# Kernel tuning notes

Hardware: AMD Instinct MI355X
Metric: run time of the kernel (lower is better)

## Reference

```python
import jax, jax.numpy as jnp
import numpy as np

M, IN, OUT, R = 8192, 4096, 4096, 16  # tokens, in_features, out_features, lora rank


def setup_inputs() -> dict:
    key = jax.random.key(0)
    k = jax.random.split(key, 7)
    # symmetric int8 quantized activations and weights
    x = jax.random.randint(k[0], (M, IN), -127, 128, dtype=jnp.int8)
    weight = jax.random.randint(k[1], (OUT, IN), -127, 128, dtype=jnp.int8)
    # per-token activation scales and per-output-channel weight scales
    x_scales = jax.random.uniform(k[2], (M,), jnp.float32, 0.5, 1.5) / 127.0
    scales = jax.random.uniform(k[3], (OUT,), jnp.float32, 0.5, 1.5) / 127.0
    bias = jax.random.normal(k[4], (OUT,), jnp.float32)
    # module inits lora_a ~ N(0, 1/r); lora_b is zeros in the module but we use
    # small random values so the LoRA path is numerically exercised
    lora_a = jax.random.normal(k[5], (R, IN), jnp.float32) * (1.0 / R)
    lora_b = jax.random.normal(k[6], (OUT, R), jnp.float32) * 0.02
    return dict(x=x, weight=weight, bias=bias, x_scales=x_scales,
                scales=scales, lora_a=lora_a, lora_b=lora_b, fuse_gelu=1)


def reference(x, weight, bias, x_scales, scales, lora_a, lora_b, fuse_gelu):
    acc = jax.lax.dot_general(x, weight, (((1,), (1,)), ((), ())),
                              preferred_element_type=jnp.int32)
    # dequantize with outer product of per-token and per-channel scales
    main = acc.astype(jnp.float32) * x_scales[:, None] * scales[None, :]
    # LoRA correction on the dequantized activations: (x_deq @ A^T) @ B^T
    x_deq = x.astype(jnp.float32) * x_scales[:, None]          # [M, IN]
    lora = (x_deq @ lora_a.T) @ lora_b.T                        # [M, R] @ [R, OUT]
    out = main + lora + bias[None, :]
    if fuse_gelu:  # static Python flag
        out = jax.nn.gelu(out, approximate=True)  # tanh-approx GELU (CUDA fused path)
    return out
```

## Files before the change

### kernel.cpp

```cpp
#include <hip/hip_runtime.h>

#define M_DIM 8192
#define IN_DIM 4096
#define OUT_DIM 4096

typedef int   v4i  __attribute__((ext_vector_type(4)));
typedef int   v16i __attribute__((ext_vector_type(16)));
typedef short v8s  __attribute__((ext_vector_type(8)));
typedef float v4f  __attribute__((ext_vector_type(4)));
typedef float v16f __attribute__((ext_vector_type(16)));

static __device__ __forceinline__ int pack4(int a, int b, int c, int d) {
    return (a & 255) | ((b & 255) << 8) | ((c & 255) << 16) | ((d & 255) << 24);
}

static __device__ __forceinline__ short f2bf(float f) {
    unsigned u = __float_as_uint(f);
    u = (u + 0x7FFFu + ((u >> 16) & 1u)) >> 16;
    return (short)u;
}

static __device__ __forceinline__ short i2bf(int v) {
    float f = (float)v;
    return (short)(__float_as_uint(f) >> 16);
}

static __device__ __forceinline__ float gelu_tanh(float u) {
    float u2 = u * u;
    float p  = fmaf(u2, 0.0356774081f, 0.7978845608f);
    float v  = u * p;
    float e  = __builtin_amdgcn_exp2f(v * 2.8853900818f);
    return u - u * __builtin_amdgcn_rcpf(e + 1.0f);
}

static __device__ __forceinline__ void async_cp16(const signed char* g, signed char* l) {
    __builtin_amdgcn_global_load_lds((const __attribute__((address_space(1))) void*)g,
                                     (__attribute__((address_space(3))) void*)l, 16, 0, 0);
}


__global__ __launch_bounds__(256) void pack_a_kernel(const float* __restrict__ la,
                                                     short* __restrict__ a16,
                                                     float* __restrict__ T) {
    const int flat = blockIdx.x * 256 + threadIdx.x;
    size_t i = (size_t)flat * 8;
    const float4* p = (const float4*)(la + i);
    float4 a = p[0], b = p[1];
    v8s o;
    o[0] = f2bf(a.x); o[1] = f2bf(a.y); o[2] = f2bf(a.z); o[3] = f2bf(a.w);
    o[4] = f2bf(b.x); o[5] = f2bf(b.y); o[6] = f2bf(b.z); o[7] = f2bf(b.w);
    *(v8s*)(a16 + i) = o;
    float4 z = {0.f, 0.f, 0.f, 0.f};
    float4* tz = (float4*)(T + (size_t)flat * 16);
    tz[0] = z; tz[1] = z; tz[2] = z; tz[3] = z;
}

__global__ __launch_bounds__(256) void pack_w_kernel(const int* __restrict__ w,
                                                     signed char* __restrict__ w8t) {
    const int flat = blockIdx.x * 256 + threadIdx.x;
    const int l  = flat & 63;
    const int gp = (flat >> 6) & 15;
    const int kk = (flat >> 10) & 63;
    const int bn = flat >> 16;
    const int n = bn * 256 + ((gp >> 1) << 5) + (l & 31);
    const int k = kk * 64 + ((gp & 1) << 5) + ((l >> 5) << 4);
    const int4* p = (const int4*)(w + (size_t)n * IN_DIM + k);
    int4 a = p[0], b = p[1], c = p[2], d = p[3];
    int4 o;
    o.x = pack4(a.x, a.y, a.z, a.w);
    o.y = pack4(b.x, b.y, b.z, b.w);
    o.z = pack4(c.x, c.y, c.z, c.w);
    o.w = pack4(d.x, d.y, d.z, d.w);
    *(int4*)(w8t + (size_t)flat * 16) = o;
}

__global__ __launch_bounds__(256) void pack_x_lora_kernel(const int* __restrict__ x,
                                                          const short* __restrict__ a16,
                                                          signed char* __restrict__ x8t,
                                                          float* __restrict__ T) {
    __shared__ float red[4 * 256];
    const int tid = threadIdx.x;
    const int lane = tid & 63, wv = tid >> 6;
    const int fr = lane & 15, fq = lane >> 4;
    const int blk = blockIdx.x;
    const int m0 = (blk >> 2) * 16;
    const int ks = blk & 3;
    const int bm = m0 >> 8;
    const int g  = (m0 >> 5) & 7;
    const int l5 = (m0 & 16) + fr;
    const int row = m0 + fr;

    v4f acc = {0.f, 0.f, 0.f, 0.f};
#pragma unroll 4
    for (int kt = 0; kt < 8; ++kt) {
        const int k  = ks * 1024 + wv * 256 + kt * 32 + fq * 8;
        const int4* xp = (const int4*)(x + (size_t)row * IN_DIM + k);
        int4 a = xp[0], b = xp[1];
        const int kk = k >> 6, c = (k >> 4) & 3, j8 = (k >> 3) & 1;
        int2 pk = make_int2(pack4(a.x, a.y, a.z, a.w), pack4(b.x, b.y, b.z, b.w));
        *(int2*)(x8t + ((size_t)((bm * 64 + kk) * 16 + g * 2 + (c >> 1))) * 1024 +
                 ((c & 1) * 32 + l5) * 16 + j8 * 8) = pk;
        v8s xa;
        xa[0] = i2bf(a.x); xa[1] = i2bf(a.y); xa[2] = i2bf(a.z); xa[3] = i2bf(a.w);
        xa[4] = i2bf(b.x); xa[5] = i2bf(b.y); xa[6] = i2bf(b.z); xa[7] = i2bf(b.w);
        v8s aa = *(const v8s*)(a16 + (size_t)fr * IN_DIM + k);
        acc = __builtin_amdgcn_mfma_f32_16x16x32_bf16(xa, aa, acc, 0, 0, 0);
    }
    *(v4f*)&red[wv * 256 + lane * 4] = acc;
    __syncthreads();

    float s = red[tid] + red[256 + tid] + red[512 + tid] + red[768 + tid];
    const int sl = tid >> 2, j = tid & 3;
    const int r16 = ((sl >> 4) << 2) + j, col = sl & 15;
    atomicAdd(&T[(size_t)(m0 + r16) * 16 + col], s);
}

__global__ __launch_bounds__(256, 2) void q8_gemm_kernel(
    const signed char* __restrict__ x8t, const signed char* __restrict__ w8t,
    const float* __restrict__ Tp, const float* __restrict__ lbm,
    const float* __restrict__ bias, const float* __restrict__ xsc,
    const float* __restrict__ wsc, const int* __restrict__ gflag,
    float* __restrict__ out) {
    __shared__ __align__(16) signed char smem[73728];

    const int tid  = threadIdx.x;
    const int lane = tid & 63;
    const int wv   = tid >> 6;
    const int wm   = wv >> 1, wn = wv & 1;
    const int b   = blockIdx.x;
    const int xcd = b & 7, rr = b >> 3;
    const int bm  = xcd * 4 + (rr & 3);
    const int bn  = rr >> 2;

    const int lofs = lane * 16;
    const size_t toff = (size_t)tid * 16;
    const signed char* Asrc = x8t + (size_t)bm * (64 * 16 * 1024);
    const signed char* Bsrc = w8t + (size_t)(bn >> 1) * (64 * 16 * 1024) + (bn & 1) * 8192;

    v16i acc[4][2];
    {
        v16i z;
#pragma unroll
        for (int i = 0; i < 16; ++i) z[i] = 0;
#pragma unroll
        for (int mt = 0; mt < 4; ++mt)
#pragma unroll
            for (int nt = 0; nt < 2; ++nt) acc[mt][nt] = z;
    }

#pragma unroll
    for (int tt = 0; tt < 2; ++tt) {
        const signed char* gA = Asrc + (size_t)tt * 16384 + toff;
        const signed char* gB = Bsrc + (size_t)tt * 16384 + toff;
        signed char* sA = smem + tt * 24576 + (wv << 10);
        signed char* sB = sA + 16384;
        async_cp16(gA,         sA);
        async_cp16(gA + 4096,  sA + 4096);
        async_cp16(gA + 8192,  sA + 8192);
        async_cp16(gA + 12288, sA + 12288);
        async_cp16(gB,         sB);
        async_cp16(gB + 4096,  sB + 4096);
    }
    asm volatile("s_waitcnt vmcnt(6)" ::: "memory");
    __builtin_amdgcn_s_barrier();

    int cur = 0;
    for (int t = 0; t < 64; ++t) {
        const signed char* Ab = smem + cur * 24576;
        const signed char* Bb = Ab + 16384;
        const int sb = (cur == 0) ? 2 : cur - 1;
        signed char* sA = smem + sb * 24576 + (wv << 10);
        signed char* sB = sA + 16384;
        const signed char* gA = Asrc + (size_t)(t + 2) * 16384 + toff;
        const signed char* gB = Bsrc + (size_t)(t + 2) * 16384 + toff;
        const bool pf = (t < 62);

        v4i a0, a1, a2, a3, b0, b1;

        a0 = *(const v4i*)(Ab + ((wm * 4 + 0) * 2 + 0) * 1024 + lofs);
        a1 = *(const v4i*)(Ab + ((wm * 4 + 1) * 2 + 0) * 1024 + lofs);
        a2 = *(const v4i*)(Ab + ((wm * 4 + 2) * 2 + 0) * 1024 + lofs);
        a3 = *(const v4i*)(Ab + ((wm * 4 + 3) * 2 + 0) * 1024 + lofs);
        b0 = *(const v4i*)(Bb + ((wn * 2 + 0) * 2 + 0) * 1024 + lofs);
        b1 = *(const v4i*)(Bb + ((wn * 2 + 1) * 2 + 0) * 1024 + lofs);
        if (pf) {
            async_cp16(gA,        sA);
            async_cp16(gA + 4096, sA + 4096);
            async_cp16(gB,        sB);
        }
        __builtin_amdgcn_s_barrier();
        __builtin_amdgcn_s_setprio(1);
        acc[0][0] = __builtin_amdgcn_mfma_i32_32x32x32_i8(a0, b0, acc[0][0], 0, 0, 0);
        acc[0][1] = __builtin_amdgcn_mfma_i32_32x32x32_i8(a0, b1, acc[0][1], 0, 0, 0);
        acc[1][0] = __builtin_amdgcn_mfma_i32_32x32x32_i8(a1, b0, acc[1][0], 0, 0, 0);
        acc[1][1] = __builtin_amdgcn_mfma_i32_32x32x32_i8(a1, b1, acc[1][1], 0, 0, 0);
        acc[2][0] = __builtin_amdgcn_mfma_i32_32x32x32_i8(a2, b0, acc[2][0], 0, 0, 0);
        acc[2][1] = __builtin_amdgcn_mfma_i32_32x32x32_i8(a2, b1, acc[2][1], 0, 0, 0);
        acc[3][0] = __builtin_amdgcn_mfma_i32_32x32x32_i8(a3, b0, acc[3][0], 0, 0, 0);
        acc[3][1] = __builtin_amdgcn_mfma_i32_32x32x32_i8(a3, b1, acc[3][1], 0, 0, 0);
        __builtin_amdgcn_s_setprio(0);

        a0 = *(const v4i*)(Ab + ((wm * 4 + 0) * 2 + 1) * 1024 + lofs);
        a1 = *(const v4i*)(Ab + ((wm * 4 + 1) * 2 + 1) * 1024 + lofs);
        a2 = *(const v4i*)(Ab + ((wm * 4 + 2) * 2 + 1) * 1024 + lofs);
        a3 = *(const v4i*)(Ab + ((wm * 4 + 3) * 2 + 1) * 1024 + lofs);
        b0 = *(const v4i*)(Bb + ((wn * 2 + 0) * 2 + 1) * 1024 + lofs);
        b1 = *(const v4i*)(Bb + ((wn * 2 + 1) * 2 + 1) * 1024 + lofs);
        if (pf) {
            async_cp16(gA + 8192,  sA + 8192);
            async_cp16(gA + 12288, sA + 12288);
            async_cp16(gB + 4096,  sB + 4096);
        }
        __builtin_amdgcn_s_barrier();
        __builtin_amdgcn_s_setprio(1);
        acc[0][0] = __builtin_amdgcn_mfma_i32_32x32x32_i8(a0, b0, acc[0][0], 0, 0, 0);
        acc[0][1] = __builtin_amdgcn_mfma_i32_32x32x32_i8(a0, b1, acc[0][1], 0, 0, 0);
        acc[1][0] = __builtin_amdgcn_mfma_i32_32x32x32_i8(a1, b0, acc[1][0], 0, 0, 0);
        acc[1][1] = __builtin_amdgcn_mfma_i32_32x32x32_i8(a1, b1, acc[1][1], 0, 0, 0);
        acc[2][0] = __builtin_amdgcn_mfma_i32_32x32x32_i8(a2, b0, acc[2][0], 0, 0, 0);
        acc[2][1] = __builtin_amdgcn_mfma_i32_32x32x32_i8(a2, b1, acc[2][1], 0, 0, 0);
        acc[3][0] = __builtin_amdgcn_mfma_i32_32x32x32_i8(a3, b0, acc[3][0], 0, 0, 0);
        acc[3][1] = __builtin_amdgcn_mfma_i32_32x32x32_i8(a3, b1, acc[3][1], 0, 0, 0);
        __builtin_amdgcn_s_setprio(0);

        if (pf) {
            asm volatile("s_waitcnt vmcnt(6)" ::: "memory");
        } else if (t == 62) {
            asm volatile("s_waitcnt vmcnt(0)" ::: "memory");
        }
        if (t < 63) __builtin_amdgcn_s_barrier();
        cur = (cur == 2) ? 0 : cur + 1;
    }

    const int mbase = bm * 256 + wm * 128;
    const int nbase = bn * 128 + wn * 64;
    const int l31 = lane & 31, lh = lane >> 5;
    const bool dg = (*gflag) != 0;

    v8s tf[4], bf[2];
#pragma unroll
    for (int mt = 0; mt < 4; ++mt) {
        const float* t0 = Tp + (size_t)(mbase + mt * 32 + l31) * 16 + lh * 8;
        v8s v;
#pragma unroll
        for (int j = 0; j < 8; ++j) v[j] = f2bf(t0[j]);
        tf[mt] = v;
    }
#pragma unroll
    for (int nt = 0; nt < 2; ++nt) {
        const float* bp = lbm + (size_t)(nbase + nt * 32 + l31) * 16 + lh * 8;
        v8s v;
#pragma unroll
        for (int j = 0; j < 8; ++j) v[j] = f2bf(bp[j]);
        bf[nt] = v;
    }
    float wsa[2], bba[2];
#pragma unroll
    for (int nt = 0; nt < 2; ++nt) {
        const int col = nbase + nt * 32 + l31;
        wsa[nt] = wsc[col];
        bba[nt] = bias[col];
    }

#pragma unroll
    for (int mt = 0; mt < 4; ++mt) {
        const int rowb = mbase + mt * 32 + lh * 4;
        float4 xs0 = *(const float4*)(xsc + rowb);
        float4 xs1 = *(const float4*)(xsc + rowb + 8);
        float4 xs2 = *(const float4*)(xsc + rowb + 16);
        float4 xs3 = *(const float4*)(xsc + rowb + 24);
        float xsv[16] = {xs0.x, xs0.y, xs0.z, xs0.w, xs1.x, xs1.y, xs1.z, xs1.w,
                         xs2.x, xs2.y, xs2.z, xs2.w, xs3.x, xs3.y, xs3.z, xs3.w};
#pragma unroll
        for (int nt = 0; nt < 2; ++nt) {
            v16f fa;
#pragma unroll
            for (int i = 0; i < 16; ++i) fa[i] = (float)acc[mt][nt][i] * wsa[nt];
            fa = __builtin_amdgcn_mfma_f32_32x32x16_bf16(tf[mt], bf[nt], fa, 0, 0, 0);
            const int col = nbase + nt * 32 + l31;
#pragma unroll
            for (int r = 0; r < 16; ++r) {
                float u = fmaf(xsv[r], fa[r], bba[nt]);
                if (dg) u = gelu_tanh(u);
                out[(size_t)(rowb + (r & 3) + 8 * (r >> 2)) * OUT_DIM + col] = u;
            }
        }
    }
}

extern "C" void kernel_launch(void* const* d_in, const int* in_sizes, int n_in,
                              void* d_out, int out_size, void* d_ws, size_t ws_size,
                              hipStream_t stream) {
    const int*   x     = (const int*)d_in[0];
    const int*   wt    = (const int*)d_in[1];
    const float* bias  = (const float*)d_in[2];
    const float* xsc   = (const float*)d_in[3];
    const float* wsc   = (const float*)d_in[4];
    const float* la    = (const float*)d_in[5];
    const float* lb    = (const float*)d_in[6];
    const int*   gflag = (const int*)d_in[7];
    float* out = (float*)d_out;

    signed char* x8t = (signed char*)d_ws;
    signed char* w8t = x8t + (size_t)M_DIM * IN_DIM;
    float* T = (float*)(w8t + (size_t)OUT_DIM * IN_DIM);
    short* a16 = (short*)w8t;

    pack_a_kernel<<<16 * IN_DIM / (8 * 256), 256, 0, stream>>>(la, a16, T);
    pack_x_lora_kernel<<<(M_DIM / 16) * 4, 256, 0, stream>>>(x, a16, x8t, T);
    pack_w_kernel<<<(size_t)OUT_DIM * IN_DIM / (16 * 256), 256, 0, stream>>>(wt, w8t);
    q8_gemm_kernel<<<(M_DIM / 256) * (OUT_DIM / 128), 256, 0, stream>>>(
        x8t, w8t, T, lb, bias, xsc, wsc, gflag, out);
}
```

Baseline: 423.9 us.

## Merge x/LoRA and weight packing into one launch, convert lora_a inline

Replaces the separate lora_a packing kernel, x-pack/LoRA kernel and weight-pack kernel with a small zeroing kernel plus one combined kernel. Blocks below 2048 pack activations and compute the LoRA projection, and the remaining blocks pack weights. lora_a is now read as fp32 and converted to bf16 inside the LoRA loop instead of being pre-packed. The aim is to cut launch overhead and let the two packing jobs overlap, at the cost of redundant fp32 reads and conversions of lora_a in every block.

Measured after the change: 418.7 us. Within noise of the previous version (-1.2%).

```diff
diff --git a/kernel.cpp b/kernel.cpp
--- a/kernel.cpp
+++ b/kernel.cpp
@@ -39,80 +39,77 @@
 }
 
 
-__global__ __launch_bounds__(256) void pack_a_kernel(const float* __restrict__ la,
-                                                     short* __restrict__ a16,
-                                                     float* __restrict__ T) {
+__global__ __launch_bounds__(256) void zero_t_kernel(float* __restrict__ T) {
     const int flat = blockIdx.x * 256 + threadIdx.x;
-    size_t i = (size_t)flat * 8;
-    const float4* p = (const float4*)(la + i);
-    float4 a = p[0], b = p[1];
-    v8s o;
-    o[0] = f2bf(a.x); o[1] = f2bf(a.y); o[2] = f2bf(a.z); o[3] = f2bf(a.w);
-    o[4] = f2bf(b.x); o[5] = f2bf(b.y); o[6] = f2bf(b.z); o[7] = f2bf(b.w);
-    *(v8s*)(a16 + i) = o;
     float4 z = {0.f, 0.f, 0.f, 0.f};
-    float4* tz = (float4*)(T + (size_t)flat * 16);
-    tz[0] = z; tz[1] = z; tz[2] = z; tz[3] = z;
-}
-
-__global__ __launch_bounds__(256) void pack_w_kernel(const int* __restrict__ w,
-                                                     signed char* __restrict__ w8t) {
-    const int flat = blockIdx.x * 256 + threadIdx.x;
-    const int l  = flat & 63;
-    const int gp = (flat >> 6) & 15;
-    const int kk = (flat >> 10) & 63;
-    const int bn = flat >> 16;
-    const int n = bn * 256 + ((gp >> 1) << 5) + (l & 31);
-    const int k = kk * 64 + ((gp & 1) << 5) + ((l >> 5) << 4);
-    const int4* p = (const int4*)(w + (size_t)n * IN_DIM + k);
-    int4 a = p[0], b = p[1], c = p[2], d = p[3];
-    int4 o;
-    o.x = pack4(a.x, a.y, a.z, a.w);
-    o.y = pack4(b.x, b.y, b.z, b.w);
-    o.z = pack4(c.x, c.y, c.z, c.w);
-    o.w = pack4(d.x, d.y, d.z, d.w);
-    *(int4*)(w8t + (size_t)flat * 16) = o;
-}
-
-__global__ __launch_bounds__(256) void pack_x_lora_kernel(const int* __restrict__ x,
-                                                          const short* __restrict__ a16,
-                                                          signed char* __restrict__ x8t,
-                                                          float* __restrict__ T) {
+    float4* tz = (float4*)(T + (size_t)flat * 8);
+    tz[0] = z; tz[1] = z;
+}
+
+__global__ __launch_bounds__(256) void pack_all_kernel(const int* __restrict__ x,
+                                                       const float* __restrict__ la,
+                                                       signed char* __restrict__ x8t,
+                                                       float* __restrict__ T,
+                                                       const int* __restrict__ w,
+                                                       signed char* __restrict__ w8t) {
     __shared__ float red[4 * 256];
+    const int b = blockIdx.x;
     const int tid = threadIdx.x;
-    const int lane = tid & 63, wv = tid >> 6;
-    const int fr = lane & 15, fq = lane >> 4;
-    const int blk = blockIdx.x;
-    const int m0 = (blk >> 2) * 16;
-    const int ks = blk & 3;
-    const int bm = m0 >> 8;
-    const int g  = (m0 >> 5) & 7;
-    const int l5 = (m0 & 16) + fr;
-    const int row = m0 + fr;
-
-    v4f acc = {0.f, 0.f, 0.f, 0.f};
+    if (b < 2048) {
+        const int lane = tid & 63, wv = tid >> 6;
+        const int fr = lane & 15, fq = lane >> 4;
+        const int m0 = (b >> 2) * 16;
+        const int ks = b & 3;
+        const int bm = m0 >> 8;
+        const int g  = (m0 >> 5) & 7;
+        const int l5 = (m0 & 16) + fr;
+        const int row = m0 + fr;
+
+        v4f acc = {0.f, 0.f, 0.f, 0.f};
 #pragma unroll 4
-    for (int kt = 0; kt < 8; ++kt) {
-        const int k  = ks * 1024 + wv * 256 + kt * 32 + fq * 8;
-        const int4* xp = (const int4*)(x + (size_t)row * IN_DIM + k);
-        int4 a = xp[0], b = xp[1];
-        const int kk = k >> 6, c = (k >> 4) & 3, j8 = (k >> 3) & 1;
-        int2 pk = make_int2(pack4(a.x, a.y, a.z, a.w), pack4(b.x, b.y, b.z, b.w));
-        *(int2*)(x8t + ((size_t)((bm * 64 + kk) * 16 + g * 2 + (c >> 1))) * 1024 +
-                 ((c & 1) * 32 + l5) * 16 + j8 * 8) = pk;
-        v8s xa;
-        xa[0] = i2bf(a.x); xa[1] = i2bf(a.y); xa[2] = i2bf(a.z); xa[3] = i2bf(a.w);
-        xa[4] = i2bf(b.x); xa[5] = i2bf(b.y); xa[6] = i2bf(b.z); xa[7] = i2bf(b.w);
-        v8s aa = *(const v8s*)(a16 + (size_t)fr * IN_DIM + k);
-        acc = __builtin_amdgcn_mfma_f32_16x16x32_bf16(xa, aa, acc, 0, 0, 0);
-    }
-    *(v4f*)&red[wv * 256 + lane * 4] = acc;
-    __syncthreads();
-
-    float s = red[tid] + red[256 + tid] + red[512 + tid] + red[768 + tid];
-    const int sl = tid >> 2, j = tid & 3;
-    const int r16 = ((sl >> 4) << 2) + j, col = sl & 15;
-    atomicAdd(&T[(size_t)(m0 + r16) * 16 + col], s);
+        for (int kt = 0; kt < 8; ++kt) {
+            const int k  = ks * 1024 + wv * 256 + kt * 32 + fq * 8;
+            const int4* xp = (const int4*)(x + (size_t)row * IN_DIM + k);
+            int4 a = xp[0], bb = xp[1];
+            const int kk = k >> 6, c = (k >> 4) & 3, j8 = (k >> 3) & 1;
+            int2 pk = make_int2(pack4(a.x, a.y, a.z, a.w), pack4(bb.x, bb.y, bb.z, bb.w));
+            *(int2*)(x8t + ((size_t)((bm * 64 + kk) * 16 + g * 2 + (c >> 1))) * 1024 +
+                     ((c & 1) * 32 + l5) * 16 + j8 * 8) = pk;
+            v8s xa;
+            xa[0] = i2bf(a.x);  xa[1] = i2bf(a.y);  xa[2] = i2bf(a.z);  xa[3] = i2bf(a.w);
+            xa[4] = i2bf(bb.x); xa[5] = i2bf(bb.y); xa[6] = i2bf(bb.z); xa[7] = i2bf(bb.w);
+            const float* ap = la + (size_t)fr * IN_DIM + k;
+            float4 af0 = *(const float4*)(ap);
+            float4 af1 = *(const float4*)(ap + 4);
+            v8s aa;
+            aa[0] = f2bf(af0.x); aa[1] = f2bf(af0.y); aa[2] = f2bf(af0.z); aa[3] = f2bf(af0.w);
+            aa[4] = f2bf(af1.x); aa[5] = f2bf(af1.y); aa[6] = f2bf(af1.z); aa[7] = f2bf(af1.w);
+            acc = __builtin_amdgcn_mfma_f32_16x16x32_bf16(xa, aa, acc, 0, 0, 0);
+        }
+        *(v4f*)&red[wv * 256 + lane * 4] = acc;
+        __syncthreads();
+
+        float s = red[tid] + red[256 + tid] + red[512 + tid] + red[768 + tid];
+        const int sl = tid >> 2, j = tid & 3;
+        const int r16 = ((sl >> 4) << 2) + j, col = sl & 15;
+        atomicAdd(&T[(size_t)(m0 + r16) * 16 + col], s);
+    } else {
+        const int flat = (b - 2048) * 256 + tid;
+        const int l  = flat & 63;
+        const int gp = (flat >> 6) & 15;
+        const int kk = (flat >> 10) & 63;
+        const int bn = flat >> 16;
+        const int n = bn * 256 + ((gp >> 1) << 5) + (l & 31);
+        const int k = kk * 64 + ((gp & 1) << 5) + ((l >> 5) << 4);
+        const int4* p = (const int4*)(w + (size_t)n * IN_DIM + k);
+        int4 a = p[0], bb = p[1], c = p[2], d = p[3];
+        int4 o;
+        o.x = pack4(a.x, a.y, a.z, a.w);
+        o.y = pack4(bb.x, bb.y, bb.z, bb.w);
+        o.z = pack4(c.x, c.y, c.z, c.w);
+        o.w = pack4(d.x, d.y, d.z, d.w);
+        *(int4*)(w8t + (size_t)flat * 16) = o;
+    }
 }
 
 __global__ __launch_bounds__(256, 2) void q8_gemm_kernel(
@@ -304,11 +301,9 @@
     signed char* x8t = (signed char*)d_ws;
     signed char* w8t = x8t + (size_t)M_DIM * IN_DIM;
     float* T = (float*)(w8t + (size_t)OUT_DIM * IN_DIM);
-    short* a16 = (short*)w8t;
-
-    pack_a_kernel<<<16 * IN_DIM / (8 * 256), 256, 0, stream>>>(la, a16, T);
-    pack_x_lora_kernel<<<(M_DIM / 16) * 4, 256, 0, stream>>>(x, a16, x8t, T);
-    pack_w_kernel<<<(size_t)OUT_DIM * IN_DIM / (16 * 256), 256, 0, stream>>>(wt, w8t);
+
+    zero_t_kernel<<<64, 256, 0, stream>>>(T);
+    pack_all_kernel<<<2048 + 4096, 256, 0, stream>>>(x, la, x8t, T, wt, w8t);
     q8_gemm_kernel<<<(M_DIM / 256) * (OUT_DIM / 128), 256, 0, stream>>>(
         x8t, w8t, T, lb, bias, xsc, wsc, gflag, out);
 }
```
